# Optimization experiments

Hardware: AMD Instinct MI355X
Metric: run time of the kernel (lower is better)

## Reference

```python
import jax, jax.numpy as jnp
import numpy as np

N_NODES = 100000
N_EDGES = 1600000
N_GRAPHS = 512


def gcn_conv(x, src, dst, W, b, num_nodes):
    """PyG GCNConv: add self-loops, sym-normalize, aggregate, add bias."""
    xw = x @ W  # [N, out]
    # degree over destination nodes, +1 for the implicit self-loop
    deg = jax.ops.segment_sum(jnp.ones(src.shape[0], xw.dtype), dst,
                              num_segments=num_nodes) + 1.0
    dinv = jax.lax.rsqrt(deg)  # deg >= 1, safe
    norm = dinv[src] * dinv[dst]  # [E]
    agg = jax.ops.segment_sum(xw[src] * norm[:, None], dst,
                              num_segments=num_nodes)
    # self-loop contribution: dinv[i]^2 * xw[i]
    agg = agg + xw * (dinv * dinv)[:, None]
    return agg + b


def global_mean_pool(x, batch, num_graphs):
    sums = jax.ops.segment_sum(x, batch, num_segments=num_graphs)
    cnts = jax.ops.segment_sum(jnp.ones(x.shape[0], x.dtype), batch,
                               num_segments=num_graphs)
    return sums / jnp.maximum(cnts, 1.0)[:, None]


def setup_inputs() -> dict:
    key = jax.random.key(0)
    ks = jax.random.split(key, 9)
    x = jax.random.normal(ks[0], (N_NODES, 3), dtype=jnp.float32)
    edge_index = jax.random.randint(ks[1], (2, N_EDGES), 0, N_NODES, dtype=jnp.int64)
    batch = jnp.sort(jax.random.randint(ks[2], (N_NODES,), 0, N_GRAPHS, dtype=jnp.int64))
    W1 = jax.random.normal(ks[3], (3, 32), dtype=jnp.float32) * 0.5
    b1 = jax.random.normal(ks[4], (32,), dtype=jnp.float32) * 0.1
    W2 = jax.random.normal(ks[5], (32, 32), dtype=jnp.float32) * 0.2
    b2 = jax.random.normal(ks[6], (32,), dtype=jnp.float32) * 0.1
    Wl = jax.random.normal(ks[7], (32, 2), dtype=jnp.float32) * 0.2
    bl = jax.random.normal(ks[8], (2,), dtype=jnp.float32) * 0.1
    return {"x": x, "edge_index": edge_index, "batch": batch,
            "W1": W1, "b1": b1, "W2": W2, "b2": b2, "Wl": Wl, "bl": bl}


def reference(x, edge_index, batch, W1, b1, W2, b2, Wl, bl):
    src, dst = edge_index[0], edge_index[1]
    h = jax.nn.relu(gcn_conv(x, src, dst, W1, b1, N_NODES))
    h = jax.nn.relu(gcn_conv(h, src, dst, W2, b2, N_NODES))
    g = global_mean_pool(h, batch, N_GRAPHS)  # [G, 32]
    return g @ Wl + bl  # [G, 2]
```

## Files before the change

kernel.cpp:

```cpp
#include <hip/hip_runtime.h>
#include <hip/hip_fp16.h>

#define NN 100000
#define NE 1600000
#define NG 512
#define F  32

#define BSH    8
#define BNODES 256
#define NB     ((NN + BNODES - 1) / BNODES)
#define CAP    5120
#define PCHUNK 4096
#define EPT    8
#define NWGP   ((NE + PCHUNK - 1) / PCHUNK)

__global__ void k_partition(const int* __restrict__ src, const int* __restrict__ dst,
                            int* __restrict__ cursor, int* __restrict__ part) {
    __shared__ int   s_cnt[NB];
    __shared__ int   s_lstart[NB];
    __shared__ int   s_base[NB];
    __shared__ int   wsum[8];
    __shared__ int   lsort[PCHUNK];
    __shared__ short lbkt[PCHUNK];
    int tid = threadIdx.x;
    for (int i = tid; i < NB; i += 512) s_cnt[i] = 0;
    __syncthreads();
    int e0 = blockIdx.x * PCHUNK;
    int e1 = min(e0 + PCHUNK, NE);
    int pk[EPT]; short bk[EPT];
    int m = 0;
#pragma unroll
    for (int k = 0; k < EPT; ++k) {
        int e = e0 + tid + k * 512;
        if (e < e1) {
            int d = dst[e];
            pk[m] = (src[e] << 8) | (d & (BNODES - 1));
            bk[m] = (short)(d >> BSH);
            atomicAdd(&s_cnt[bk[m]], 1);
            ++m;
        }
    }
    __syncthreads();
    int cv = (tid < NB) ? s_cnt[tid] : 0;
    int v = cv;
#pragma unroll
    for (int o = 1; o < 64; o <<= 1) {
        int t = __shfl_up(v, o, 64);
        if ((tid & 63) >= o) v += t;
    }
    if ((tid & 63) == 63) wsum[tid >> 6] = v;
    __syncthreads();
    int add = 0;
    for (int w = 0; w < (tid >> 6); ++w) add += wsum[w];
    int excl = v + add - cv;
    if (tid < NB) {
        s_lstart[tid] = excl;
        if (cv) s_base[tid] = tid * CAP + atomicAdd(&cursor[tid], cv);
        s_cnt[tid] = 0;
    }
    __syncthreads();
    for (int k = 0; k < m; ++k) {
        int b = bk[k];
        int r = s_lstart[b] + atomicAdd(&s_cnt[b], 1);
        lsort[r] = pk[k];
        lbkt[r]  = (short)b;
    }
    __syncthreads();
    int cnt = e1 - e0;
    for (int i = tid; i < cnt; i += 512) {
        int b = lbkt[i];
        part[s_base[b] + (i - s_lstart[b])] = lsort[i];
    }
}

__global__ void k_fill2a(const int* __restrict__ part, const int* __restrict__ cursor,
                         const float* __restrict__ x,
                         int* __restrict__ rowpack, float* __restrict__ dinv,
                         float4* __restrict__ xd) {
    __shared__ int cnt[BNODES];
    __shared__ int wsum[4];
    int b = blockIdx.x, tid = threadIdx.x;
    int node0 = b << BSH;
    int s0 = b * CAP, s1 = s0 + cursor[b];
    cnt[tid] = 0;
    __syncthreads();
    for (int i = s0 + tid; i < s1; i += 256) atomicAdd(&cnt[part[i] & (BNODES - 1)], 1);
    __syncthreads();
    int c = cnt[tid];
    int v = c;
#pragma unroll
    for (int o = 1; o < 64; o <<= 1) {
        int t = __shfl_up(v, o, 64);
        if ((tid & 63) >= o) v += t;
    }
    if ((tid & 63) == 63) wsum[tid >> 6] = v;
    __syncthreads();
    int add = 0;
    for (int w = 0; w < (tid >> 6); ++w) add += wsum[w];
    int excl = v + add - c;
    int n = node0 + tid;
    if (n < NN) {
        rowpack[n] = ((s0 + excl) << 10) | c;
        float d = rsqrtf((float)c + 1.0f);
        dinv[n] = d;
        xd[n] = make_float4(d * x[n * 3 + 0], d * x[n * 3 + 1], d * x[n * 3 + 2], d);
    }
}

__global__ void k_fill2b(const int* __restrict__ part, const int* __restrict__ cursor,
                         const int* __restrict__ rowpack, const float4* __restrict__ xd,
                         const float* __restrict__ W1, const float* __restrict__ b1,
                         int* __restrict__ csr, __half2* __restrict__ g1) {
    __shared__ int lcsr[CAP];
    __shared__ int off[BNODES];
    __shared__ float W1s[3 * F];
    __shared__ float b1s[F];
    int b = blockIdx.x, tid = threadIdx.x;
    int node0 = b << BSH;
    int s0 = b * CAP;
    int cnt = cursor[b];
    if (tid < 3 * F) W1s[tid] = W1[tid];
    if (tid < F) b1s[tid] = b1[tid];
    int n = node0 + tid;
    int pack = (n < NN) ? rowpack[n] : (s0 << 10);
    off[tid] = (pack >> 10) - s0;
    __syncthreads();
    for (int i = tid; i < cnt; i += 256) {
        int p = part[s0 + i];
        int pos = atomicAdd(&off[p & (BNODES - 1)], 1);
        lcsr[pos] = p >> 8;
    }
    __syncthreads();
    for (int i = tid; i < cnt; i += 256) csr[s0 + i] = lcsr[i];
    if (n < NN) {
        int deg = pack & 1023;
        int beg = (pack >> 10) - s0;
        int end = beg + deg;
        float ax = 0.0f, ay = 0.0f, az = 0.0f;
        int e = beg;
        for (; e + 7 < end; e += 8) {
#pragma unroll
            for (int u = 0; u < 8; ++u) {
                float4 v = xd[lcsr[e + u]];
                ax += v.x; ay += v.y; az += v.z;
            }
        }
        for (; e < end; ++e) {
            float4 v = xd[lcsr[e]];
            ax += v.x; ay += v.y; az += v.z;
        }
        float4 sf = xd[n];
        float dn = sf.w;
        float cx = dn * (ax + sf.x), cy = dn * (ay + sf.y), cz = dn * (az + sf.z);
        __half2 tmp[16];
#pragma unroll
        for (int j = 0; j < 16; ++j) {
            int f0 = 2 * j, f1 = 2 * j + 1;
            float v0 = cx * W1s[f0] + cy * W1s[F + f0] + cz * W1s[2 * F + f0] + b1s[f0];
            float v1 = cx * W1s[f1] + cy * W1s[F + f1] + cz * W1s[2 * F + f1] + b1s[f1];
            tmp[j] = __floats2half2_rn(dn * fmaxf(v0, 0.0f), dn * fmaxf(v1, 0.0f));
        }
        uint4* hv = (uint4*)(g1 + (size_t)n * 16);
        const uint4* tv = (const uint4*)tmp;
        hv[0] = tv[0]; hv[1] = tv[1]; hv[2] = tv[2]; hv[3] = tv[3];
    }
}

__global__ void k_gather2p(const int* __restrict__ rowpack, const int* __restrict__ csr,
                           const __half2* __restrict__ g1, const float* __restrict__ dinv,
                           const int* __restrict__ batch,
                           const float* __restrict__ W2, const float* __restrict__ b2,
                           float* __restrict__ gsum) {
    __shared__ float W2s[F * F];
    __shared__ float b2s[F];
    __shared__ float ts[16][F];
    __shared__ float hs[16][F];
    __shared__ int bat[16];
    int tid = threadIdx.x;
    int nb = blockIdx.x * 16;
    for (int i = tid; i < F * F; i += 256) W2s[i] = W2[i];
    if (tid < F) b2s[tid] = b2[tid];
    if (tid < 16) bat[tid] = batch[nb + tid];
    int nl = tid >> 4, j = tid & 15;
    int n = nb + nl;
    {
        int pack = rowpack[n];
        int beg = pack >> 10, end = beg + (pack & 1023);
        float ax = 0.0f, ay = 0.0f;
        int e = beg;
        for (; e + 7 < end; e += 8) {
            int s0 = csr[e],     s1 = csr[e + 1], s2 = csr[e + 2], s3 = csr[e + 3];
            int s4 = csr[e + 4], s5 = csr[e + 5], s6 = csr[e + 6], s7 = csr[e + 7];
            float2 v0 = __half22float2(g1[s0 * 16 + j]);
            float2 v1 = __half22float2(g1[s1 * 16 + j]);
            float2 v2 = __half22float2(g1[s2 * 16 + j]);
            float2 v3 = __half22float2(g1[s3 * 16 + j]);
            float2 v4 = __half22float2(g1[s4 * 16 + j]);
            float2 v5 = __half22float2(g1[s5 * 16 + j]);
            float2 v6 = __half22float2(g1[s6 * 16 + j]);
            float2 v7 = __half22float2(g1[s7 * 16 + j]);
            ax += ((v0.x + v1.x) + (v2.x + v3.x)) + ((v4.x + v5.x) + (v6.x + v7.x));
            ay += ((v0.y + v1.y) + (v2.y + v3.y)) + ((v4.y + v5.y) + (v6.y + v7.y));
        }
        for (; e + 3 < end; e += 4) {
            int s0 = csr[e], s1 = csr[e + 1], s2 = csr[e + 2], s3 = csr[e + 3];
            float2 v0 = __half22float2(g1[s0 * 16 + j]);
            float2 v1 = __half22float2(g1[s1 * 16 + j]);
            float2 v2 = __half22float2(g1[s2 * 16 + j]);
            float2 v3 = __half22float2(g1[s3 * 16 + j]);
            ax += (v0.x + v1.x) + (v2.x + v3.x);
            ay += (v0.y + v1.y) + (v2.y + v3.y);
        }
        for (; e < end; ++e) {
            float2 v = __half22float2(g1[csr[e] * 16 + j]);
            ax += v.x; ay += v.y;
        }
        float dn = dinv[n];
        float2 sf = __half22float2(g1[n * 16 + j]);
        ts[nl][2 * j]     = dn * (ax + sf.x);
        ts[nl][2 * j + 1] = dn * (ay + sf.y);
    }
    __syncthreads();
    {
        int f = tid & 31;
        int nn0 = tid >> 5;
#pragma unroll
        for (int pass = 0; pass < 2; ++pass) {
            int nn = nn0 + pass * 8;
            float acc = b2s[f];
#pragma unroll
            for (int k = 0; k < F; ++k) acc += ts[nn][k] * W2s[k * F + f];
            hs[nn][f] = fmaxf(acc, 0.0f);
        }
    }
    __syncthreads();
    if (tid < F) {
        int g0 = bat[0], gmax = bat[15];
        for (int g = g0; g <= gmax; ++g) {
            float s = 0.0f;
#pragma unroll
            for (int i = 0; i < 16; ++i) if (bat[i] == g) s += hs[i][tid];
            atomicAdd(&gsum[g * F + tid], s);
        }
    }
}

__global__ void k_head(const float* __restrict__ gsum, const int* __restrict__ batch,
                       const float* __restrict__ Wl, const float* __restrict__ bl,
                       float* __restrict__ out) {
    int g = blockIdx.x * blockDim.x + threadIdx.x;
    if (g >= NG) return;
    int lo = 0, hi = NN;
    while (lo < hi) { int m = (lo + hi) >> 1; if (batch[m] < g) lo = m + 1; else hi = m; }
    int s = lo;
    lo = 0; hi = NN;
    while (lo < hi) { int m = (lo + hi) >> 1; if (batch[m] < g + 1) lo = m + 1; else hi = m; }
    float inv = 1.0f / fmaxf((float)(lo - s), 1.0f);
    float a0 = 0.0f, a1 = 0.0f;
#pragma unroll
    for (int k = 0; k < F; ++k) {
        float m = gsum[g * F + k] * inv;
        a0 += m * Wl[k * 2 + 0];
        a1 += m * Wl[k * 2 + 1];
    }
    out[g * 2 + 0] = a0 + bl[0];
    out[g * 2 + 1] = a1 + bl[1];
}

extern "C" void kernel_launch(void* const* d_in, const int* in_sizes, int n_in,
                              void* d_out, int out_size, void* d_ws, size_t ws_size,
                              hipStream_t stream) {
    const float* x     = (const float*)d_in[0];
    const int*   eidx  = (const int*)d_in[1];
    const int*   batch = (const int*)d_in[2];
    const float* W1    = (const float*)d_in[3];
    const float* b1    = (const float*)d_in[4];
    const float* W2    = (const float*)d_in[5];
    const float* b2    = (const float*)d_in[6];
    const float* Wl    = (const float*)d_in[7];
    const float* bl    = (const float*)d_in[8];
    float*       out   = (float*)d_out;

    const int* src = eidx;
    const int* dst = eidx + NE;

    char* base = (char*)d_ws;
    size_t off = 0;
    auto alloc = [&](size_t bytes) {
        void* p = base + off;
        off = (off + bytes + 127) & ~(size_t)127;
        return p;
    };
    int*     cursor  = (int*)alloc(NB * sizeof(int) + (size_t)NG * F * sizeof(float));
    float*   gsum    = (float*)(cursor + NB);
    int*     rowpack = (int*)alloc(NN * sizeof(int));
    int*     part    = (int*)alloc((size_t)NB * CAP * sizeof(int));
    int*     csr     = (int*)alloc((size_t)NB * CAP * sizeof(int));
    float*   dinv    = (float*)alloc(NN * sizeof(float));
    float4*  xd      = (float4*)alloc(NN * sizeof(float4));
    __half2* g1      = (__half2*)alloc((size_t)NN * 16 * sizeof(__half2));

    const int B = 256;
    const int gG16 = NN / 16;

    hipMemsetAsync(cursor, 0, NB * sizeof(int) + (size_t)NG * F * sizeof(float), stream);

    k_partition<<<NWGP, 512, 0, stream>>>(src, dst, cursor, part);
    k_fill2a   <<<NB,   B,   0, stream>>>(part, cursor, x, rowpack, dinv, xd);
    k_fill2b   <<<NB,   B,   0, stream>>>(part, cursor, rowpack, xd, W1, b1, csr, g1);

    k_gather2p<<<gG16, B, 0, stream>>>(rowpack, csr, g1, dinv, batch, W2, b2, gsum);

    k_head<<<(NG + B - 1) / B, B, 0, stream>>>(gsum, batch, Wl, bl, out);
}
```

Before: 165.3 us.

## Replace bucket partition CSR build with global-atomic degree count and scatter

Drops the shared-memory bucket partition plus the per-bucket local CSR fill. It now counts degrees with global atomics, scans per 256-node block, and scatters src into the CSR with per-node atomic cursors. In the same edge pass it accumulates the layer-1 aggregation with float atomics. This removes the intermediate part buffer and one pass over it, at the cost of about 1.6M times 4 random global atomics and non-deterministic CSR order and float summation.

New measurement: 506.4 us. 206% more time.

```diff
diff --git a/kernel.cpp b/kernel.cpp
--- a/kernel.cpp
+++ b/kernel.cpp
@@ -10,39 +10,29 @@
 #define BNODES 256
 #define NB     ((NN + BNODES - 1) / BNODES)
 #define CAP    5120
-#define PCHUNK 4096
-#define EPT    8
-#define NWGP   ((NE + PCHUNK - 1) / PCHUNK)
-
-__global__ void k_partition(const int* __restrict__ src, const int* __restrict__ dst,
-                            int* __restrict__ cursor, int* __restrict__ part) {
-    __shared__ int   s_cnt[NB];
-    __shared__ int   s_lstart[NB];
-    __shared__ int   s_base[NB];
-    __shared__ int   wsum[8];
-    __shared__ int   lsort[PCHUNK];
-    __shared__ short lbkt[PCHUNK];
-    int tid = threadIdx.x;
-    for (int i = tid; i < NB; i += 512) s_cnt[i] = 0;
-    __syncthreads();
-    int e0 = blockIdx.x * PCHUNK;
-    int e1 = min(e0 + PCHUNK, NE);
-    int pk[EPT]; short bk[EPT];
-    int m = 0;
-#pragma unroll
-    for (int k = 0; k < EPT; ++k) {
-        int e = e0 + tid + k * 512;
-        if (e < e1) {
-            int d = dst[e];
-            pk[m] = (src[e] << 8) | (d & (BNODES - 1));
-            bk[m] = (short)(d >> BSH);
-            atomicAdd(&s_cnt[bk[m]], 1);
-            ++m;
-        }
-    }
-    __syncthreads();
-    int cv = (tid < NB) ? s_cnt[tid] : 0;
-    int v = cv;
+
+__global__ void k_deg(const int* __restrict__ dst, int* __restrict__ deg) {
+    int t = blockIdx.x * blockDim.x + threadIdx.x;
+    int e = t * 4;
+    if (e + 3 < NE) {
+        int4 d = *(const int4*)(dst + e);
+        atomicAdd(&deg[d.x], 1);
+        atomicAdd(&deg[d.y], 1);
+        atomicAdd(&deg[d.z], 1);
+        atomicAdd(&deg[d.w], 1);
+    } else {
+        for (; e < NE; ++e) atomicAdd(&deg[dst[e]], 1);
+    }
+}
+
+__global__ void k_nodeinit(const int* __restrict__ deg, const float* __restrict__ x,
+                           int* __restrict__ rowpack, int* __restrict__ wcur,
+                           float* __restrict__ dinv, float4* __restrict__ xd) {
+    __shared__ int wsum[4];
+    int b = blockIdx.x, tid = threadIdx.x;
+    int n = (b << BSH) + tid;
+    int c = (n < NN) ? deg[n] : 0;
+    int v = c;
 #pragma unroll
     for (int o = 1; o < 64; o <<= 1) {
         int t = __shfl_up(v, o, 64);
@@ -52,118 +42,97 @@
     __syncthreads();
     int add = 0;
     for (int w = 0; w < (tid >> 6); ++w) add += wsum[w];
-    int excl = v + add - cv;
-    if (tid < NB) {
-        s_lstart[tid] = excl;
-        if (cv) s_base[tid] = tid * CAP + atomicAdd(&cursor[tid], cv);
-        s_cnt[tid] = 0;
-    }
-    __syncthreads();
-    for (int k = 0; k < m; ++k) {
-        int b = bk[k];
-        int r = s_lstart[b] + atomicAdd(&s_cnt[b], 1);
-        lsort[r] = pk[k];
-        lbkt[r]  = (short)b;
-    }
-    __syncthreads();
-    int cnt = e1 - e0;
-    for (int i = tid; i < cnt; i += 512) {
-        int b = lbkt[i];
-        part[s_base[b] + (i - s_lstart[b])] = lsort[i];
-    }
-}
-
-__global__ void k_fill2a(const int* __restrict__ part, const int* __restrict__ cursor,
-                         const float* __restrict__ x,
-                         int* __restrict__ rowpack, float* __restrict__ dinv,
-                         float4* __restrict__ xd) {
-    __shared__ int cnt[BNODES];
-    __shared__ int wsum[4];
-    int b = blockIdx.x, tid = threadIdx.x;
-    int node0 = b << BSH;
-    int s0 = b * CAP, s1 = s0 + cursor[b];
-    cnt[tid] = 0;
-    __syncthreads();
-    for (int i = s0 + tid; i < s1; i += 256) atomicAdd(&cnt[part[i] & (BNODES - 1)], 1);
-    __syncthreads();
-    int c = cnt[tid];
-    int v = c;
-#pragma unroll
-    for (int o = 1; o < 64; o <<= 1) {
-        int t = __shfl_up(v, o, 64);
-        if ((tid & 63) >= o) v += t;
-    }
-    if ((tid & 63) == 63) wsum[tid >> 6] = v;
-    __syncthreads();
-    int add = 0;
-    for (int w = 0; w < (tid >> 6); ++w) add += wsum[w];
     int excl = v + add - c;
-    int n = node0 + tid;
     if (n < NN) {
-        rowpack[n] = ((s0 + excl) << 10) | c;
+        int pos = b * CAP + excl;
+        rowpack[n] = (pos << 10) | c;
+        wcur[n] = pos;
         float d = rsqrtf((float)c + 1.0f);
         dinv[n] = d;
         xd[n] = make_float4(d * x[n * 3 + 0], d * x[n * 3 + 1], d * x[n * 3 + 2], d);
     }
 }
 
-__global__ void k_fill2b(const int* __restrict__ part, const int* __restrict__ cursor,
-                         const int* __restrict__ rowpack, const float4* __restrict__ xd,
-                         const float* __restrict__ W1, const float* __restrict__ b1,
-                         int* __restrict__ csr, __half2* __restrict__ g1) {
-    __shared__ int lcsr[CAP];
-    __shared__ int off[BNODES];
+__global__ void k_edge(const int* __restrict__ src, const int* __restrict__ dst,
+                       const float4* __restrict__ xd,
+                       int* __restrict__ wcur, int* __restrict__ csr,
+                       float* __restrict__ agg) {
+    int t = blockIdx.x * blockDim.x + threadIdx.x;
+    int e = t * 4;
+    if (e + 3 < NE) {
+        int4 s = *(const int4*)(src + e);
+        int4 d = *(const int4*)(dst + e);
+        {
+            float4 v = xd[s.x];
+            int p = atomicAdd(&wcur[d.x], 1);
+            csr[p] = s.x;
+            atomicAdd(&agg[4 * d.x + 0], v.x);
+            atomicAdd(&agg[4 * d.x + 1], v.y);
+            atomicAdd(&agg[4 * d.x + 2], v.z);
+        }
+        {
+            float4 v = xd[s.y];
+            int p = atomicAdd(&wcur[d.y], 1);
+            csr[p] = s.y;
+            atomicAdd(&agg[4 * d.y + 0], v.x);
+            atomicAdd(&agg[4 * d.y + 1], v.y);
+            atomicAdd(&agg[4 * d.y + 2], v.z);
+        }
+        {
+            float4 v = xd[s.z];
+            int p = atomicAdd(&wcur[d.z], 1);
+            csr[p] = s.z;
+            atomicAdd(&agg[4 * d.z + 0], v.x);
+            atomicAdd(&agg[4 * d.z + 1], v.y);
+            atomicAdd(&agg[4 * d.z + 2], v.z);
+        }
+        {
+            float4 v = xd[s.w];
+            int p = atomicAdd(&wcur[d.w], 1);
+            csr[p] = s.w;
+            atomicAdd(&agg[4 * d.w + 0], v.x);
+            atomicAdd(&agg[4 * d.w + 1], v.y);
+            atomicAdd(&agg[4 * d.w + 2], v.z);
+        }
+    } else {
+        for (; e < NE; ++e) {
+            int sv = src[e], dv = dst[e];
+            float4 v = xd[sv];
+            int p = atomicAdd(&wcur[dv], 1);
+            csr[p] = sv;
+            atomicAdd(&agg[4 * dv + 0], v.x);
+            atomicAdd(&agg[4 * dv + 1], v.y);
+            atomicAdd(&agg[4 * dv + 2], v.z);
+        }
+    }
+}
+
+__global__ void k_l1(const float4* __restrict__ aggv, const float4* __restrict__ xd,
+                     const float* __restrict__ W1, const float* __restrict__ b1,
+                     __half2* __restrict__ g1) {
     __shared__ float W1s[3 * F];
     __shared__ float b1s[F];
-    int b = blockIdx.x, tid = threadIdx.x;
-    int node0 = b << BSH;
-    int s0 = b * CAP;
-    int cnt = cursor[b];
+    int tid = threadIdx.x;
     if (tid < 3 * F) W1s[tid] = W1[tid];
     if (tid < F) b1s[tid] = b1[tid];
-    int n = node0 + tid;
-    int pack = (n < NN) ? rowpack[n] : (s0 << 10);
-    off[tid] = (pack >> 10) - s0;
-    __syncthreads();
-    for (int i = tid; i < cnt; i += 256) {
-        int p = part[s0 + i];
-        int pos = atomicAdd(&off[p & (BNODES - 1)], 1);
-        lcsr[pos] = p >> 8;
-    }
-    __syncthreads();
-    for (int i = tid; i < cnt; i += 256) csr[s0 + i] = lcsr[i];
-    if (n < NN) {
-        int deg = pack & 1023;
-        int beg = (pack >> 10) - s0;
-        int end = beg + deg;
-        float ax = 0.0f, ay = 0.0f, az = 0.0f;
-        int e = beg;
-        for (; e + 7 < end; e += 8) {
-#pragma unroll
-            for (int u = 0; u < 8; ++u) {
-                float4 v = xd[lcsr[e + u]];
-                ax += v.x; ay += v.y; az += v.z;
-            }
-        }
-        for (; e < end; ++e) {
-            float4 v = xd[lcsr[e]];
-            ax += v.x; ay += v.y; az += v.z;
-        }
-        float4 sf = xd[n];
-        float dn = sf.w;
-        float cx = dn * (ax + sf.x), cy = dn * (ay + sf.y), cz = dn * (az + sf.z);
-        __half2 tmp[16];
-#pragma unroll
-        for (int j = 0; j < 16; ++j) {
-            int f0 = 2 * j, f1 = 2 * j + 1;
-            float v0 = cx * W1s[f0] + cy * W1s[F + f0] + cz * W1s[2 * F + f0] + b1s[f0];
-            float v1 = cx * W1s[f1] + cy * W1s[F + f1] + cz * W1s[2 * F + f1] + b1s[f1];
-            tmp[j] = __floats2half2_rn(dn * fmaxf(v0, 0.0f), dn * fmaxf(v1, 0.0f));
-        }
-        uint4* hv = (uint4*)(g1 + (size_t)n * 16);
-        const uint4* tv = (const uint4*)tmp;
-        hv[0] = tv[0]; hv[1] = tv[1]; hv[2] = tv[2]; hv[3] = tv[3];
-    }
+    __syncthreads();
+    int n = blockIdx.x * 256 + tid;
+    if (n >= NN) return;
+    float4 a = aggv[n];
+    float4 sf = xd[n];
+    float dn = sf.w;
+    float cx = dn * (a.x + sf.x), cy = dn * (a.y + sf.y), cz = dn * (a.z + sf.z);
+    __half2 tmp[16];
+#pragma unroll
+    for (int j = 0; j < 16; ++j) {
+        int f0 = 2 * j, f1 = 2 * j + 1;
+        float v0 = cx * W1s[f0] + cy * W1s[F + f0] + cz * W1s[2 * F + f0] + b1s[f0];
+        float v1 = cx * W1s[f1] + cy * W1s[F + f1] + cz * W1s[2 * F + f1] + b1s[f1];
+        tmp[j] = __floats2half2_rn(dn * fmaxf(v0, 0.0f), dn * fmaxf(v1, 0.0f));
+    }
+    uint4* hv = (uint4*)(g1 + (size_t)n * 16);
+    const uint4* tv = (const uint4*)tmp;
+    hv[0] = tv[0]; hv[1] = tv[1]; hv[2] = tv[2]; hv[3] = tv[3];
 }
 
 __global__ void k_gather2p(const int* __restrict__ rowpack, const int* __restrict__ csr,
@@ -291,23 +260,28 @@
         off = (off + bytes + 127) & ~(size_t)127;
         return p;
     };
-    int*     cursor  = (int*)alloc(NB * sizeof(int) + (size_t)NG * F * sizeof(float));
-    float*   gsum    = (float*)(cursor + NB);
-    int*     rowpack = (int*)alloc(NN * sizeof(int));
-    int*     part    = (int*)alloc((size_t)NB * CAP * sizeof(int));
-    int*     csr     = (int*)alloc((size_t)NB * CAP * sizeof(int));
-    float*   dinv    = (float*)alloc(NN * sizeof(float));
-    float4*  xd      = (float4*)alloc(NN * sizeof(float4));
-    __half2* g1      = (__half2*)alloc((size_t)NN * 16 * sizeof(__half2));
+    size_t zbytes = (size_t)NN * sizeof(int) + (size_t)NG * F * sizeof(float)
+                  + (size_t)NN * 4 * sizeof(float);
+    int*    deg  = (int*)alloc(zbytes);
+    float*  gsum = (float*)(deg + NN);
+    float*  agg  = gsum + (size_t)NG * F;
+    int*    rowpack = (int*)alloc(NN * sizeof(int));
+    int*    wcur    = (int*)alloc(NN * sizeof(int));
+    float*  dinv    = (float*)alloc(NN * sizeof(float));
+    float4* xd      = (float4*)alloc(NN * sizeof(float4));
+    int*    csr     = (int*)alloc((size_t)NB * CAP * sizeof(int));
+    __half2* g1     = (__half2*)alloc((size_t)NN * 16 * sizeof(__half2));
 
     const int B = 256;
+    const int gE4  = (NE / 4 + B - 1) / B;
     const int gG16 = NN / 16;
 
-    hipMemsetAsync(cursor, 0, NB * sizeof(int) + (size_t)NG * F * sizeof(float), stream);
-
-    k_partition<<<NWGP, 512, 0, stream>>>(src, dst, cursor, part);
-    k_fill2a   <<<NB,   B,   0, stream>>>(part, cursor, x, rowpack, dinv, xd);
-    k_fill2b   <<<NB,   B,   0, stream>>>(part, cursor, rowpack, xd, W1, b1, csr, g1);
+    hipMemsetAsync(deg, 0, zbytes, stream);
+
+    k_deg     <<<gE4, B, 0, stream>>>(dst, deg);
+    k_nodeinit<<<NB,  B, 0, stream>>>(deg, x, rowpack, wcur, dinv, xd);
+    k_edge    <<<gE4, B, 0, stream>>>(src, dst, xd, wcur, csr, agg);
+    k_l1      <<<NB,  B, 0, stream>>>((const float4*)agg, xd, W1, b1, g1);
 
     k_gather2p<<<gG16, B, 0, stream>>>(rowpack, csr, g1, dinv, batch, W2, b2, gsum);
 
```
